# Optimization experiments

Hardware: AMD Instinct MI355X
Metric: run time of the kernel (lower is better)

Reference implementation:

```python
import jax, jax.numpy as jnp
import numpy as np

B = 32768
C = 1000


def setup_inputs() -> dict:
    key = jax.random.key(0)
    k1, k2, k3 = jax.random.split(key, 3)
    output = jax.random.normal(k1, (B, C), dtype=jnp.float32)
    target = jax.random.randint(k2, (B,), 0, C, dtype=jnp.int64)
    # loss_lams rows are (approx) probability vectors from the previous epoch
    lams = jax.random.uniform(k3, (C, C), dtype=jnp.float32)
    loss_lams = lams / jnp.sum(lams, axis=1, keepdims=True)
    return {"output": output, "target": target, "loss_lams": loss_lams}


def reference(output, target, loss_lams):
    """OLS loss forward.

    Returns (loss, cur_epoch_lams_update, cur_epoch_cnt_update) where the
    updates are the increments added to the zero-initialized per-epoch state
    (update_loss_lams side effect), and loss = 0.5*CE + 0.5*softCE.
    """
    b, c = output.shape
    target = target.astype(jnp.int32)

    # --- update_loss_lams: softmax, keep samples where argmax == target,
    # scatter-add their prob vectors into the row of their target class ---
    probs = jax.nn.softmax(output, axis=1)                      # [B, C]
    pred = jnp.argmax(probs, axis=1)                            # [B]
    correct = (pred == target).astype(output.dtype)             # [B]
    lams_update = jax.ops.segment_sum(probs * correct[:, None], target,
                                      num_segments=c)           # [C, C]
    cnt_update = jax.ops.segment_sum(correct, target, num_segments=c)  # [C]

    # --- loss: 0.5 * hard CE + 0.5 * soft CE with loss_lams soft labels ---
    log_probs = jax.nn.log_softmax(output, axis=1)              # [B, C]
    ce = -jnp.mean(jnp.take_along_axis(log_probs, target[:, None], axis=1))
    soft_targets = loss_lams[target]                            # [B, C] gather
    soft_ce = -jnp.sum(log_probs * soft_targets) / b
    loss = 0.5 * ce + 0.5 * soft_ce
    return loss, lams_update, cnt_update
```

## Files before the change

### kernel.cpp

```cpp
#include <hip/hip_runtime.h>
#include <math.h>

constexpr int B_ROWS = 32768;
constexpr int C_COLS = 1000;
constexpr int VEC4   = C_COLS / 4;
constexpr int NBLK   = 2048;
constexpr int NWAVE  = NBLK * 4;

using f4 = __attribute__((ext_vector_type(4))) float;

__global__ __launch_bounds__(256) void ols_main(
    const float* __restrict__ output,
    const int*   __restrict__ target,
    const float* __restrict__ lams,
    float*       __restrict__ partials,
    float*       __restrict__ lams_upd,
    float*       __restrict__ cnt_upd)
{
    __shared__ float s_loss[4];
    const int lane  = threadIdx.x & 63;
    const int wid   = threadIdx.x >> 6;
    const int gwave = blockIdx.x * 4 + wid;
    const bool has3 = lane < (VEC4 - 192);

    float lossAcc = 0.0f;

#pragma unroll 1
    for (int i = 0; i < 4; ++i) {
        const int row = gwave + i * NWAVE;

        const int t = target[row];

        const f4* xr = reinterpret_cast<const f4*>(output + (size_t)row * C_COLS);
        f4 v0 = xr[lane];
        f4 v1 = xr[lane + 64];
        f4 v2 = xr[lane + 128];
        f4 v3 = has3 ? xr[lane + 192] : (f4){-INFINITY, -INFINITY, -INFINITY, -INFINITY};

        const f4* lr = reinterpret_cast<const f4*>(lams + (size_t)t * C_COLS);
        f4 l0 = lr[lane];
        f4 l1 = lr[lane + 64];
        f4 l2 = lr[lane + 128];
        f4 l3 = has3 ? lr[lane + 192] : (f4){0.0f, 0.0f, 0.0f, 0.0f};

        float m  = v0[0];
        int   am = 4 * lane;
#define OLS_UPD(val, idx) { float _v = (val); if (_v > m) { m = _v; am = (idx); } }
        OLS_UPD(v0[1], 4*lane + 1)   OLS_UPD(v0[2], 4*lane + 2)   OLS_UPD(v0[3], 4*lane + 3)
        OLS_UPD(v1[0], 4*lane + 256) OLS_UPD(v1[1], 4*lane + 257)
        OLS_UPD(v1[2], 4*lane + 258) OLS_UPD(v1[3], 4*lane + 259)
        OLS_UPD(v2[0], 4*lane + 512) OLS_UPD(v2[1], 4*lane + 513)
        OLS_UPD(v2[2], 4*lane + 514) OLS_UPD(v2[3], 4*lane + 515)
        OLS_UPD(v3[0], 4*lane + 768) OLS_UPD(v3[1], 4*lane + 769)
        OLS_UPD(v3[2], 4*lane + 770) OLS_UPD(v3[3], 4*lane + 771)
#undef OLS_UPD

#pragma unroll
        for (int off = 32; off > 0; off >>= 1) {
            float om = __shfl_xor(m, off);
            int   oa = __shfl_xor(am, off);
            if (om > m || (om == m && oa < am)) { m = om; am = oa; }
        }

        float dot = l0[0]*v0[0] + l0[1]*v0[1] + l0[2]*v0[2] + l0[3]*v0[3]
                  + l1[0]*v1[0] + l1[1]*v1[1] + l1[2]*v1[2] + l1[3]*v1[3]
                  + l2[0]*v2[0] + l2[1]*v2[1] + l2[2]*v2[2] + l2[3]*v2[3];
        float rs  = l0[0] + l0[1] + l0[2] + l0[3]
                  + l1[0] + l1[1] + l1[2] + l1[3]
                  + l2[0] + l2[1] + l2[2] + l2[3];
        if (has3) {
            dot += l3[0]*v3[0] + l3[1]*v3[1] + l3[2]*v3[2] + l3[3]*v3[3];
            rs  += l3[0] + l3[1] + l3[2] + l3[3];
        }

        float s =
            __expf(v0[0] - m) + __expf(v0[1] - m) + __expf(v0[2] - m) + __expf(v0[3] - m) +
            __expf(v1[0] - m) + __expf(v1[1] - m) + __expf(v1[2] - m) + __expf(v1[3] - m) +
            __expf(v2[0] - m) + __expf(v2[1] - m) + __expf(v2[2] - m) + __expf(v2[3] - m) +
            __expf(v3[0] - m) + __expf(v3[1] - m) + __expf(v3[2] - m) + __expf(v3[3] - m);

#pragma unroll
        for (int off = 32; off > 0; off >>= 1) {
            s   += __shfl_xor(s,   off);
            dot += __shfl_xor(dot, off);
            rs  += __shfl_xor(rs,  off);
        }

        const float lse = m + __logf(s);

        const int g = t >> 8, e = t & 3, src_lane = (t >> 2) & 63;
        f4 vg = (g == 0) ? v0 : (g == 1) ? v1 : (g == 2) ? v2 : v3;
        float ce = (e == 0) ? vg[0] : (e == 1) ? vg[1] : (e == 2) ? vg[2] : vg[3];
        const float x_t = __shfl(ce, src_lane, 64);

        lossAcc += 0.5f * ((lse - x_t) + (lse * rs - dot));

        if (am == t) {
            const float inv = 1.0f / s;
            float* dst = lams_upd + (size_t)t * C_COLS;
            atomicAdd(&dst[4*lane + 0],   __expf(v0[0] - m) * inv);
            atomicAdd(&dst[4*lane + 1],   __expf(v0[1] - m) * inv);
            atomicAdd(&dst[4*lane + 2],   __expf(v0[2] - m) * inv);
            atomicAdd(&dst[4*lane + 3],   __expf(v0[3] - m) * inv);
            atomicAdd(&dst[4*lane + 256], __expf(v1[0] - m) * inv);
            atomicAdd(&dst[4*lane + 257], __expf(v1[1] - m) * inv);
            atomicAdd(&dst[4*lane + 258], __expf(v1[2] - m) * inv);
            atomicAdd(&dst[4*lane + 259], __expf(v1[3] - m) * inv);
            atomicAdd(&dst[4*lane + 512], __expf(v2[0] - m) * inv);
            atomicAdd(&dst[4*lane + 513], __expf(v2[1] - m) * inv);
            atomicAdd(&dst[4*lane + 514], __expf(v2[2] - m) * inv);
            atomicAdd(&dst[4*lane + 515], __expf(v2[3] - m) * inv);
            if (has3) {
                atomicAdd(&dst[4*lane + 768], __expf(v3[0] - m) * inv);
                atomicAdd(&dst[4*lane + 769], __expf(v3[1] - m) * inv);
                atomicAdd(&dst[4*lane + 770], __expf(v3[2] - m) * inv);
                atomicAdd(&dst[4*lane + 771], __expf(v3[3] - m) * inv);
            }
            if (lane == 0) atomicAdd(&cnt_upd[t], 1.0f);
        }
    }

    if (lane == 0) s_loss[wid] = lossAcc;
    __syncthreads();
    if (threadIdx.x == 0)
        partials[blockIdx.x] = (s_loss[0] + s_loss[1]) + (s_loss[2] + s_loss[3]);
}

__global__ __launch_bounds__(256) void ols_reduce(
    const float* __restrict__ partials, float* __restrict__ d_loss)
{
    __shared__ float s[4];
    const int lane = threadIdx.x & 63;
    const int wid  = threadIdx.x >> 6;
    float acc = 0.0f;
#pragma unroll
    for (int i = 0; i < 8; ++i) acc += partials[threadIdx.x + i * 256];
#pragma unroll
    for (int off = 32; off > 0; off >>= 1) acc += __shfl_xor(acc, off);
    if (lane == 0) s[wid] = acc;
    __syncthreads();
    if (threadIdx.x == 0)
        *d_loss = ((s[0] + s[1]) + (s[2] + s[3])) * (1.0f / (float)B_ROWS);
}

extern "C" void kernel_launch(void* const* d_in, const int* in_sizes, int n_in,
                              void* d_out, int out_size, void* d_ws, size_t ws_size,
                              hipStream_t stream) {
    const float* output = (const float*)d_in[0];
    const int*   target = (const int*)d_in[1];
    const float* lams   = (const float*)d_in[2];

    float* out      = (float*)d_out;
    float* d_loss   = out;
    float* lams_upd = out + 1;
    float* cnt_upd  = out + 1 + C_COLS * C_COLS;
    float* partials = (float*)d_ws;

    hipMemsetAsync(d_out, 0, (size_t)out_size * sizeof(float), stream);

    ols_main<<<dim3(NBLK), dim3(256), 0, stream>>>(output, target, lams,
                                                   partials, lams_upd, cnt_upd);
    ols_reduce<<<dim3(1), dim3(256), 0, stream>>>(partials, d_loss);
}
```

Measured before the change: 202.9 us.

## Process two rows per iteration and replace argmax tracking with max comparison

New measurement: 198.9 us. About the same (-1.9%).

```diff
diff --git a/kernel.cpp b/kernel.cpp
--- a/kernel.cpp
+++ b/kernel.cpp
@@ -9,7 +9,7 @@
 
 using f4 = __attribute__((ext_vector_type(4))) float;
 
-__global__ __launch_bounds__(256) void ols_main(
+__global__ __launch_bounds__(256, 4) void ols_main(
     const float* __restrict__ output,
     const int*   __restrict__ target,
     const float* __restrict__ lams,
@@ -25,59 +25,35 @@
 
     float lossAcc = 0.0f;
 
-#pragma unroll 1
-    for (int i = 0; i < 4; ++i) {
-        const int row = gwave + i * NWAVE;
+    auto process = [&](int t,
+                       const f4& v0, const f4& v1, const f4& v2, const f4& v3,
+                       const f4& l0, const f4& l1, const f4& l2, const f4& l3) {
+        float ma = fmaxf(fmaxf(v0[0], v0[1]), fmaxf(v0[2], v0[3]));
+        float mb = fmaxf(fmaxf(v1[0], v1[1]), fmaxf(v1[2], v1[3]));
+        float mc = fmaxf(fmaxf(v2[0], v2[1]), fmaxf(v2[2], v2[3]));
+        float md = fmaxf(fmaxf(v3[0], v3[1]), fmaxf(v3[2], v3[3]));
+        float m  = fmaxf(fmaxf(ma, mb), fmaxf(mc, md));
+#pragma unroll
+        for (int off = 32; off > 0; off >>= 1) m = fmaxf(m, __shfl_xor(m, off));
 
-        const int t = target[row];
-
-        const f4* xr = reinterpret_cast<const f4*>(output + (size_t)row * C_COLS);
-        f4 v0 = xr[lane];
-        f4 v1 = xr[lane + 64];
-        f4 v2 = xr[lane + 128];
-        f4 v3 = has3 ? xr[lane + 192] : (f4){-INFINITY, -INFINITY, -INFINITY, -INFINITY};
-
-        const f4* lr = reinterpret_cast<const f4*>(lams + (size_t)t * C_COLS);
-        f4 l0 = lr[lane];
-        f4 l1 = lr[lane + 64];
-        f4 l2 = lr[lane + 128];
-        f4 l3 = has3 ? lr[lane + 192] : (f4){0.0f, 0.0f, 0.0f, 0.0f};
-
-        float m  = v0[0];
-        int   am = 4 * lane;
-#define OLS_UPD(val, idx) { float _v = (val); if (_v > m) { m = _v; am = (idx); } }
-        OLS_UPD(v0[1], 4*lane + 1)   OLS_UPD(v0[2], 4*lane + 2)   OLS_UPD(v0[3], 4*lane + 3)
-        OLS_UPD(v1[0], 4*lane + 256) OLS_UPD(v1[1], 4*lane + 257)
-        OLS_UPD(v1[2], 4*lane + 258) OLS_UPD(v1[3], 4*lane + 259)
-        OLS_UPD(v2[0], 4*lane + 512) OLS_UPD(v2[1], 4*lane + 513)
-        OLS_UPD(v2[2], 4*lane + 514) OLS_UPD(v2[3], 4*lane + 515)
-        OLS_UPD(v3[0], 4*lane + 768) OLS_UPD(v3[1], 4*lane + 769)
-        OLS_UPD(v3[2], 4*lane + 770) OLS_UPD(v3[3], 4*lane + 771)
-#undef OLS_UPD
-
-#pragma unroll
-        for (int off = 32; off > 0; off >>= 1) {
-            float om = __shfl_xor(m, off);
-            int   oa = __shfl_xor(am, off);
-            if (om > m || (om == m && oa < am)) { m = om; am = oa; }
+        float d0 = (l0[0]*v0[0] + l0[1]*v0[1]) + (l0[2]*v0[2] + l0[3]*v0[3]);
+        float d1 = (l1[0]*v1[0] + l1[1]*v1[1]) + (l1[2]*v1[2] + l1[3]*v1[3]);
+        float d2 = (l2[0]*v2[0] + l2[1]*v2[1]) + (l2[2]*v2[2] + l2[3]*v2[3]);
+        float dot = (d0 + d1) + d2;
+        float r0 = (l0[0] + l0[1]) + (l0[2] + l0[3]);
+        float r1 = (l1[0] + l1[1]) + (l1[2] + l1[3]);
+        float r2 = (l2[0] + l2[1]) + (l2[2] + l2[3]);
+        float rs = (r0 + r1) + r2;
+        if (has3) {
+            dot += (l3[0]*v3[0] + l3[1]*v3[1]) + (l3[2]*v3[2] + l3[3]*v3[3]);
+            rs  += (l3[0] + l3[1]) + (l3[2] + l3[3]);
         }
 
-        float dot = l0[0]*v0[0] + l0[1]*v0[1] + l0[2]*v0[2] + l0[3]*v0[3]
-                  + l1[0]*v1[0] + l1[1]*v1[1] + l1[2]*v1[2] + l1[3]*v1[3]
-                  + l2[0]*v2[0] + l2[1]*v2[1] + l2[2]*v2[2] + l2[3]*v2[3];
-        float rs  = l0[0] + l0[1] + l0[2] + l0[3]
-                  + l1[0] + l1[1] + l1[2] + l1[3]
-                  + l2[0] + l2[1] + l2[2] + l2[3];
-        if (has3) {
-            dot += l3[0]*v3[0] + l3[1]*v3[1] + l3[2]*v3[2] + l3[3]*v3[3];
-            rs  += l3[0] + l3[1] + l3[2] + l3[3];
-        }
-
-        float s =
-            __expf(v0[0] - m) + __expf(v0[1] - m) + __expf(v0[2] - m) + __expf(v0[3] - m) +
-            __expf(v1[0] - m) + __expf(v1[1] - m) + __expf(v1[2] - m) + __expf(v1[3] - m) +
-            __expf(v2[0] - m) + __expf(v2[1] - m) + __expf(v2[2] - m) + __expf(v2[3] - m) +
-            __expf(v3[0] - m) + __expf(v3[1] - m) + __expf(v3[2] - m) + __expf(v3[3] - m);
+        float e0 = (__expf(v0[0]-m) + __expf(v0[1]-m)) + (__expf(v0[2]-m) + __expf(v0[3]-m));
+        float e1 = (__expf(v1[0]-m) + __expf(v1[1]-m)) + (__expf(v1[2]-m) + __expf(v1[3]-m));
+        float e2 = (__expf(v2[0]-m) + __expf(v2[1]-m)) + (__expf(v2[2]-m) + __expf(v2[3]-m));
+        float e3 = (__expf(v3[0]-m) + __expf(v3[1]-m)) + (__expf(v3[2]-m) + __expf(v3[3]-m));
+        float s  = (e0 + e1) + (e2 + e3);
 
 #pragma unroll
         for (int off = 32; off > 0; off >>= 1) {
@@ -95,7 +71,7 @@
 
         lossAcc += 0.5f * ((lse - x_t) + (lse * rs - dot));
 
-        if (am == t) {
+        if (x_t == m) {
             const float inv = 1.0f / s;
             float* dst = lams_upd + (size_t)t * C_COLS;
             atomicAdd(&dst[4*lane + 0],   __expf(v0[0] - m) * inv);
@@ -118,6 +94,34 @@
             }
             if (lane == 0) atomicAdd(&cnt_upd[t], 1.0f);
         }
+    };
+
+#pragma unroll 1
+    for (int p = 0; p < 2; ++p) {
+        const int rowA = gwave + (2 * p) * NWAVE;
+        const int rowB = rowA + NWAVE;
+
+        const int tA = target[rowA];
+        const int tB = target[rowB];
+
+        const f4* xrA = reinterpret_cast<const f4*>(output + (size_t)rowA * C_COLS);
+        const f4* xrB = reinterpret_cast<const f4*>(output + (size_t)rowB * C_COLS);
+        f4 vA0 = xrA[lane];       f4 vB0 = xrB[lane];
+        f4 vA1 = xrA[lane + 64];  f4 vB1 = xrB[lane + 64];
+        f4 vA2 = xrA[lane + 128]; f4 vB2 = xrB[lane + 128];
+        f4 vA3 = has3 ? xrA[lane + 192] : (f4){-INFINITY, -INFINITY, -INFINITY, -INFINITY};
+        f4 vB3 = has3 ? xrB[lane + 192] : (f4){-INFINITY, -INFINITY, -INFINITY, -INFINITY};
+
+        const f4* lrA = reinterpret_cast<const f4*>(lams + (size_t)tA * C_COLS);
+        const f4* lrB = reinterpret_cast<const f4*>(lams + (size_t)tB * C_COLS);
+        f4 lA0 = lrA[lane];       f4 lB0 = lrB[lane];
+        f4 lA1 = lrA[lane + 64];  f4 lB1 = lrB[lane + 64];
+        f4 lA2 = lrA[lane + 128]; f4 lB2 = lrB[lane + 128];
+        f4 lA3 = has3 ? lrA[lane + 192] : (f4){0.0f, 0.0f, 0.0f, 0.0f};
+        f4 lB3 = has3 ? lrB[lane + 192] : (f4){0.0f, 0.0f, 0.0f, 0.0f};
+
+        process(tA, vA0, vA1, vA2, vA3, lA0, lA1, lA2, lA3);
+        process(tB, vB0, vB1, vB2, vB3, lB0, lB1, lB2, lB3);
     }
 
     if (lane == 0) s_loss[wid] = lossAcc;
```

## Map one row per 256-thread block instead of one row per wave

Applied to the files above, without the earlier changes.

Result: no change. 202.2 us (-0.3%).

```diff
diff --git a/kernel.cpp b/kernel.cpp
--- a/kernel.cpp
+++ b/kernel.cpp
@@ -4,12 +4,10 @@
 constexpr int B_ROWS = 32768;
 constexpr int C_COLS = 1000;
 constexpr int VEC4   = C_COLS / 4;
-constexpr int NBLK   = 2048;
-constexpr int NWAVE  = NBLK * 4;
 
 using f4 = __attribute__((ext_vector_type(4))) float;
 
-__global__ __launch_bounds__(256) void ols_main(
+__global__ __launch_bounds__(256, 8) void ols_main(
     const float* __restrict__ output,
     const int*   __restrict__ target,
     const float* __restrict__ lams,
@@ -17,130 +15,91 @@
     float*       __restrict__ lams_upd,
     float*       __restrict__ cnt_upd)
 {
-    __shared__ float s_loss[4];
-    const int lane  = threadIdx.x & 63;
-    const int wid   = threadIdx.x >> 6;
-    const int gwave = blockIdx.x * 4 + wid;
-    const bool has3 = lane < (VEC4 - 192);
+    __shared__ float s_max[4];
+    __shared__ float s_red[4][3];
+    __shared__ float s_xt;
 
-    float lossAcc = 0.0f;
+    const int tid  = threadIdx.x;
+    const int lane = tid & 63;
+    const int wid  = tid >> 6;
+    const int row  = blockIdx.x;
+    const bool act = tid < VEC4;
 
-#pragma unroll 1
-    for (int i = 0; i < 4; ++i) {
-        const int row = gwave + i * NWAVE;
+    const int t = target[row];
 
-        const int t = target[row];
+    f4 x = act ? reinterpret_cast<const f4*>(output + (size_t)row * C_COLS)[tid]
+               : (f4){-INFINITY, -INFINITY, -INFINITY, -INFINITY};
+    f4 l = act ? reinterpret_cast<const f4*>(lams + (size_t)t * C_COLS)[tid]
+               : (f4){0.0f, 0.0f, 0.0f, 0.0f};
 
-        const f4* xr = reinterpret_cast<const f4*>(output + (size_t)row * C_COLS);
-        f4 v0 = xr[lane];
-        f4 v1 = xr[lane + 64];
-        f4 v2 = xr[lane + 128];
-        f4 v3 = has3 ? xr[lane + 192] : (f4){-INFINITY, -INFINITY, -INFINITY, -INFINITY};
+    float m = fmaxf(fmaxf(x[0], x[1]), fmaxf(x[2], x[3]));
+#pragma unroll
+    for (int off = 32; off > 0; off >>= 1) m = fmaxf(m, __shfl_xor(m, off));
+    if (lane == 0) s_max[wid] = m;
 
-        const f4* lr = reinterpret_cast<const f4*>(lams + (size_t)t * C_COLS);
-        f4 l0 = lr[lane];
-        f4 l1 = lr[lane + 64];
-        f4 l2 = lr[lane + 128];
-        f4 l3 = has3 ? lr[lane + 192] : (f4){0.0f, 0.0f, 0.0f, 0.0f};
+    const int q = t >> 2, e = t & 3;
+    if (tid == q)
+        s_xt = (e == 0) ? x[0] : (e == 1) ? x[1] : (e == 2) ? x[2] : x[3];
+    __syncthreads();
 
-        float m  = v0[0];
-        int   am = 4 * lane;
-#define OLS_UPD(val, idx) { float _v = (val); if (_v > m) { m = _v; am = (idx); } }
-        OLS_UPD(v0[1], 4*lane + 1)   OLS_UPD(v0[2], 4*lane + 2)   OLS_UPD(v0[3], 4*lane + 3)
-        OLS_UPD(v1[0], 4*lane + 256) OLS_UPD(v1[1], 4*lane + 257)
-        OLS_UPD(v1[2], 4*lane + 258) OLS_UPD(v1[3], 4*lane + 259)
-        OLS_UPD(v2[0], 4*lane + 512) OLS_UPD(v2[1], 4*lane + 513)
-        OLS_UPD(v2[2], 4*lane + 514) OLS_UPD(v2[3], 4*lane + 515)
-        OLS_UPD(v3[0], 4*lane + 768) OLS_UPD(v3[1], 4*lane + 769)
-        OLS_UPD(v3[2], 4*lane + 770) OLS_UPD(v3[3], 4*lane + 771)
-#undef OLS_UPD
+    m = fmaxf(fmaxf(s_max[0], s_max[1]), fmaxf(s_max[2], s_max[3]));
+    const float x_t = s_xt;
 
+    float p0 = __expf(x[0] - m), p1 = __expf(x[1] - m);
+    float p2 = __expf(x[2] - m), p3 = __expf(x[3] - m);
+    float s   = (p0 + p1) + (p2 + p3);
+    float dot = act ? (l[0]*x[0] + l[1]*x[1]) + (l[2]*x[2] + l[3]*x[3]) : 0.0f;
+    float rs  = (l[0] + l[1]) + (l[2] + l[3]);
 #pragma unroll
-        for (int off = 32; off > 0; off >>= 1) {
-            float om = __shfl_xor(m, off);
-            int   oa = __shfl_xor(am, off);
-            if (om > m || (om == m && oa < am)) { m = om; am = oa; }
-        }
+    for (int off = 32; off > 0; off >>= 1) {
+        s   += __shfl_xor(s,   off);
+        dot += __shfl_xor(dot, off);
+        rs  += __shfl_xor(rs,  off);
+    }
+    if (lane == 0) { s_red[wid][0] = s; s_red[wid][1] = dot; s_red[wid][2] = rs; }
+    __syncthreads();
 
-        float dot = l0[0]*v0[0] + l0[1]*v0[1] + l0[2]*v0[2] + l0[3]*v0[3]
-                  + l1[0]*v1[0] + l1[1]*v1[1] + l1[2]*v1[2] + l1[3]*v1[3]
-                  + l2[0]*v2[0] + l2[1]*v2[1] + l2[2]*v2[2] + l2[3]*v2[3];
-        float rs  = l0[0] + l0[1] + l0[2] + l0[3]
-                  + l1[0] + l1[1] + l1[2] + l1[3]
-                  + l2[0] + l2[1] + l2[2] + l2[3];
-        if (has3) {
-            dot += l3[0]*v3[0] + l3[1]*v3[1] + l3[2]*v3[2] + l3[3]*v3[3];
-            rs  += l3[0] + l3[1] + l3[2] + l3[3];
-        }
+    s = (s_red[0][0] + s_red[1][0]) + (s_red[2][0] + s_red[3][0]);
 
-        float s =
-            __expf(v0[0] - m) + __expf(v0[1] - m) + __expf(v0[2] - m) + __expf(v0[3] - m) +
-            __expf(v1[0] - m) + __expf(v1[1] - m) + __expf(v1[2] - m) + __expf(v1[3] - m) +
-            __expf(v2[0] - m) + __expf(v2[1] - m) + __expf(v2[2] - m) + __expf(v2[3] - m) +
-            __expf(v3[0] - m) + __expf(v3[1] - m) + __expf(v3[2] - m) + __expf(v3[3] - m);
-
-#pragma unroll
-        for (int off = 32; off > 0; off >>= 1) {
-            s   += __shfl_xor(s,   off);
-            dot += __shfl_xor(dot, off);
-            rs  += __shfl_xor(rs,  off);
-        }
-
+    if (tid == 0) {
+        const float dT = (s_red[0][1] + s_red[1][1]) + (s_red[2][1] + s_red[3][1]);
+        const float rT = (s_red[0][2] + s_red[1][2]) + (s_red[2][2] + s_red[3][2]);
         const float lse = m + __logf(s);
-
-        const int g = t >> 8, e = t & 3, src_lane = (t >> 2) & 63;
-        f4 vg = (g == 0) ? v0 : (g == 1) ? v1 : (g == 2) ? v2 : v3;
-        float ce = (e == 0) ? vg[0] : (e == 1) ? vg[1] : (e == 2) ? vg[2] : vg[3];
-        const float x_t = __shfl(ce, src_lane, 64);
-
-        lossAcc += 0.5f * ((lse - x_t) + (lse * rs - dot));
-
-        if (am == t) {
-            const float inv = 1.0f / s;
-            float* dst = lams_upd + (size_t)t * C_COLS;
-            atomicAdd(&dst[4*lane + 0],   __expf(v0[0] - m) * inv);
-            atomicAdd(&dst[4*lane + 1],   __expf(v0[1] - m) * inv);
-            atomicAdd(&dst[4*lane + 2],   __expf(v0[2] - m) * inv);
-            atomicAdd(&dst[4*lane + 3],   __expf(v0[3] - m) * inv);
-            atomicAdd(&dst[4*lane + 256], __expf(v1[0] - m) * inv);
-            atomicAdd(&dst[4*lane + 257], __expf(v1[1] - m) * inv);
-            atomicAdd(&dst[4*lane + 258], __expf(v1[2] - m) * inv);
-            atomicAdd(&dst[4*lane + 259], __expf(v1[3] - m) * inv);
-            atomicAdd(&dst[4*lane + 512], __expf(v2[0] - m) * inv);
-            atomicAdd(&dst[4*lane + 513], __expf(v2[1] - m) * inv);
-            atomicAdd(&dst[4*lane + 514], __expf(v2[2] - m) * inv);
-            atomicAdd(&dst[4*lane + 515], __expf(v2[3] - m) * inv);
-            if (has3) {
-                atomicAdd(&dst[4*lane + 768], __expf(v3[0] - m) * inv);
-                atomicAdd(&dst[4*lane + 769], __expf(v3[1] - m) * inv);
-                atomicAdd(&dst[4*lane + 770], __expf(v3[2] - m) * inv);
-                atomicAdd(&dst[4*lane + 771], __expf(v3[3] - m) * inv);
-            }
-            if (lane == 0) atomicAdd(&cnt_upd[t], 1.0f);
-        }
+        partials[row] = 0.5f * ((lse - x_t) + (lse * rT - dT));
     }
 
-    if (lane == 0) s_loss[wid] = lossAcc;
-    __syncthreads();
-    if (threadIdx.x == 0)
-        partials[blockIdx.x] = (s_loss[0] + s_loss[1]) + (s_loss[2] + s_loss[3]);
+    if (x_t == m) {
+        const float inv = 1.0f / s;
+        if (act) {
+            float* dst = lams_upd + (size_t)t * C_COLS + 4 * tid;
+            atomicAdd(dst + 0, p0 * inv);
+            atomicAdd(dst + 1, p1 * inv);
+            atomicAdd(dst + 2, p2 * inv);
+            atomicAdd(dst + 3, p3 * inv);
+        }
+        if (tid == 0) atomicAdd(&cnt_upd[t], 1.0f);
+    }
 }
 
 __global__ __launch_bounds__(256) void ols_reduce(
     const float* __restrict__ partials, float* __restrict__ d_loss)
 {
-    __shared__ float s[4];
+    __shared__ float sm[4];
     const int lane = threadIdx.x & 63;
     const int wid  = threadIdx.x >> 6;
+    const f4* p4 = reinterpret_cast<const f4*>(partials);
     float acc = 0.0f;
 #pragma unroll
-    for (int i = 0; i < 8; ++i) acc += partials[threadIdx.x + i * 256];
+    for (int k = 0; k < 32; ++k) {
+        f4 v = p4[threadIdx.x + k * 256];
+        acc += (v[0] + v[1]) + (v[2] + v[3]);
+    }
 #pragma unroll
     for (int off = 32; off > 0; off >>= 1) acc += __shfl_xor(acc, off);
-    if (lane == 0) s[wid] = acc;
+    if (lane == 0) sm[wid] = acc;
     __syncthreads();
     if (threadIdx.x == 0)
-        *d_loss = ((s[0] + s[1]) + (s[2] + s[3])) * (1.0f / (float)B_ROWS);
+        *d_loss = ((sm[0] + sm[1]) + (sm[2] + sm[3])) * (1.0f / (float)B_ROWS);
 }
 
 extern "C" void kernel_launch(void* const* d_in, const int* in_sizes, int n_in,
@@ -158,7 +117,7 @@
 
     hipMemsetAsync(d_out, 0, (size_t)out_size * sizeof(float), stream);
 
-    ols_main<<<dim3(NBLK), dim3(256), 0, stream>>>(output, target, lams,
-                                                   partials, lams_upd, cnt_upd);
+    ols_main<<<dim3(B_ROWS), dim3(256), 0, stream>>>(output, target, lams,
+                                                     partials, lams_upd, cnt_upd);
     ols_reduce<<<dim3(1), dim3(256), 0, stream>>>(partials, d_loss);
 }
```
